# Kernel optimization log

Measured on AMD Instinct MI355X. Metric: run time of the kernel, lower is better.

Reference implementation:

```python
import jax, jax.numpy as jnp
import numpy as np

DILATIONS = (1, 2, 4, 8, 16, 32, 64, 128, 256, 512)
K = 3            # kernel_size
CH = 128         # channels
B, T = 4, 16384
L = len(DILATIONS)


def _conv1x1(x, w, b=None):
    # x: [B, Cin, T], w: [Cout, Cin, 1] -> [B, Cout, T]
    y = jnp.einsum('oc,bct->bot', w[..., 0], x)
    return y if b is None else y + b[None, :, None]


def _causal_dilated_conv(x, w, b, d):
    # buffer of zeros of size (K-1)*d concatenated on the left == causal left pad
    pad = (K - 1) * d
    y = jax.lax.conv_general_dilated(
        x, w, window_strides=(1,), padding=[(pad, 0)], rhs_dilation=(d,),
        dimension_numbers=('NCH', 'OIH', 'NCH'))
    return y + b[None, :, None]


def setup_inputs() -> dict:
    key = jax.random.key(0)
    ks = jax.random.split(key, 12)
    s = 0.1  # keep gated activations out of saturation
    return {
        'x': jax.random.normal(ks[0], (B, 1, T), jnp.float32),
        'c': jax.random.normal(ks[1], (B, 1, T), jnp.float32),
        'head_init': jnp.zeros((B, CH, T), jnp.float32),
        'w_re': jax.random.normal(ks[2], (CH, 1, 1), jnp.float32) * s,
        'conv_w': jax.random.normal(ks[3], (L, 2 * CH, CH, K), jnp.float32) * s,
        'conv_b': jax.random.normal(ks[4], (L, 2 * CH), jnp.float32) * s,
        'mix_w': jax.random.normal(ks[5], (L, 2 * CH, 1, 1), jnp.float32) * s,
        'w1x1': jax.random.normal(ks[6], (L, CH, CH, 1), jnp.float32) * s,
        'b1x1': jax.random.normal(ks[7], (L, CH), jnp.float32) * s,
        'w_head': jax.random.normal(ks[8], (1, CH, 1), jnp.float32) * s,
        'b_head': jax.random.normal(ks[9], (1,), jnp.float32) * s,
    }


def reference(x, c, head_init, w_re, conv_w, conv_b, mix_w, w1x1, b1x1, w_head, b_head):
    h = _conv1x1(x, w_re)               # rechannel: [B, CH, T]
    head = head_init                    # head accumulator (zeros == head_input=None)
    for li, d in enumerate(DILATIONS):  # fixed small layer loop (structurally distinct dilations)
        z = _causal_dilated_conv(h, conv_w[li], conv_b[li], d)   # [B, 2CH, T]
        z = z + _conv1x1(c, mix_w[li])                           # conditioning mixer
        post = jnp.tanh(z[:, :CH]) * jax.nn.sigmoid(z[:, CH:])   # gated activation
        h = h + _conv1x1(post, w1x1[li], b1x1[li])               # residual
        head = head + post
    out = _conv1x1(head, w_head, b_head)  # [B, 1, T]
    return out, h
```

## Files before the change

kernel.cpp:

```cpp
#include <hip/hip_runtime.h>
#include <hip/hip_bf16.h>

#define B_   4
#define T_   16384
#define CH_  128
#define TCH_ 256
#define NL_  10
#define TT_  64
#define SHW_ 196
#define SPW_ 68

typedef __attribute__((ext_vector_type(8))) short short8;
typedef __attribute__((ext_vector_type(4))) float f32x4;

#define MFMA16(a, b, c) __builtin_amdgcn_mfma_f32_16x16x32_bf16(a, b, c, 0, 0, 0)

__device__ __forceinline__ unsigned short f2bf(float f) {
  unsigned u = __float_as_uint(f);
  return (unsigned short)((u + 0x7FFFu + ((u >> 16) & 1u)) >> 16);
}
__device__ __forceinline__ float bf2f(unsigned s) {
  return __uint_as_float((s & 0xFFFFu) << 16);
}
__device__ __forceinline__ float fast_tanh(float x) {
  float e = __expf(2.0f * fabsf(x));
  float t = 1.0f - 2.0f / (e + 1.0f);
  return copysignf(t, x);
}
__device__ __forceinline__ float fast_sig(float x) {
  return 1.0f / (1.0f + __expf(-x));
}

__global__ __launch_bounds__(256) void pack_w(
    const float* __restrict__ conv_w, const float* __restrict__ w1x1,
    unsigned short* __restrict__ wpackA, unsigned short* __restrict__ wpack1) {
  const int NA = NL_ * 4 * 4 * 12 * 64 * 8;
  int idx = blockIdx.x * 256 + threadIdx.x;
  if (idx < NA) {
    int j = idx & 7;
    int t1 = idx >> 3;
    int l = t1 & 63;
    int t2 = t1 >> 6;
    int ks = t2 % 12;
    int t3 = t2 / 12;
    int f = t3 & 3;
    int t4 = t3 >> 2;
    int w = t4 & 3;
    int li = t4 >> 2;
    int o = 32 * w + 16 * (f & 1) + 128 * (f >> 1) + (l & 15);
    int ck = 32 * ks + 8 * (l >> 4) + j;
    int c = ck & 127, k = ck >> 7;
    wpackA[idx] = f2bf(conv_w[((li * TCH_ + o) * CH_ + c) * 3 + k]);
  } else {
    int i2 = idx - NA;
    if (i2 < NL_ * 4 * 2 * 4 * 64 * 8) {
      int j = i2 & 7;
      int t1 = i2 >> 3;
      int l = t1 & 63;
      int t2 = t1 >> 6;
      int ks = t2 & 3;
      int t3 = t2 >> 2;
      int p = t3 & 1;
      int t4 = t3 >> 1;
      int w = t4 & 3;
      int li = t4 >> 2;
      int o = 32 * w + 16 * p + (l & 15);
      int c = 32 * ks + 8 * (l >> 4) + j;
      wpack1[i2] = f2bf(w1x1[(li * CH_ + o) * CH_ + c]);
    }
  }
}

__global__ __launch_bounds__(256) void rechannel_k(
    const float* __restrict__ x, const float* __restrict__ w_re,
    unsigned short* __restrict__ hb) {
  int flat = blockIdx.x * 256 + threadIdx.x;
  int cid = flat & 15;
  int t = (flat >> 4) & (T_ - 1);
  int b = flat >> 18;
  float xv = x[b * T_ + t];
  const float* wr = w_re + cid * 8;
  union { short8 s; unsigned short u[8]; } o;
#pragma unroll
  for (int j = 0; j < 8; ++j) o.u[j] = f2bf(wr[j] * xv);
  *(short8*)(hb + (size_t)(b * T_ + t) * CH_ + cid * 8) = o.s;
}

__global__ __launch_bounds__(256) void out_init_k(
    const float* __restrict__ head_init, const float* __restrict__ w_head,
    const float* __restrict__ b_head, float* __restrict__ out) {
  int idx = blockIdx.x * 256 + threadIdx.x;
  int b = idx / T_;
  int t = idx - b * T_;
  float acc = b_head[0];
#pragma unroll 8
  for (int c = 0; c < CH_; ++c)
    acc += w_head[c] * head_init[(b * CH_ + c) * T_ + t];
  out[idx] = acc;
}

__global__ __launch_bounds__(256, 2) void layer_k(
    const unsigned short* __restrict__ hin,
    unsigned short* __restrict__ hob,
    float* __restrict__ hof,
    const float* __restrict__ cin, float* __restrict__ out,
    const unsigned short* __restrict__ wA,
    const unsigned short* __restrict__ w1p,
    const float* __restrict__ bconv,
    const float* __restrict__ wmix,
    const float* __restrict__ b1,
    const float* __restrict__ w_head,
    int d, int is_final) {
  __shared__ unsigned shH[TT_ * SHW_];
  __shared__ unsigned shP[TT_ * SPW_];
  __shared__ float shR[4 * 4 * 16];

  const int tid = threadIdx.x;
  const int b = blockIdx.y;
  const int t0 = blockIdx.x * TT_;

#pragma unroll
  for (int it = 0; it < 12; ++it) {
    int flat = it * 256 + tid;
    int cid = flat & 15;
    int tt = (flat >> 4) & 63;
    int k = flat >> 10;
    int t = t0 + tt - (2 - k) * d;
    uint4 v = make_uint4(0u, 0u, 0u, 0u);
    if (t >= 0)
      v = *(const uint4*)(hin + ((size_t)(b * T_ + t) * CH_ + cid * 8));
    *(uint4*)(shH + tt * SHW_ + k * 64 + cid * 4) = v;
  }
  __syncthreads();

  const int wave = __builtin_amdgcn_readfirstlane(tid >> 6);
  const int lane = tid & 63;
  const int r = lane & 15;
  const int g = lane >> 4;

  f32x4 accL[2][4], accH[2][4];
#pragma unroll
  for (int p = 0; p < 2; ++p)
#pragma unroll
    for (int q = 0; q < 4; ++q) {
      accL[p][q] = (f32x4){0.f, 0.f, 0.f, 0.f};
      accH[p][q] = (f32x4){0.f, 0.f, 0.f, 0.f};
    }

  const short8* wAv = (const short8*)wA;
#pragma unroll
  for (int ks = 0; ks < 12; ++ks) {
    short8 bf[4];
#pragma unroll
    for (int q = 0; q < 4; ++q)
      bf[q] = *(const short8*)(shH + (16 * q + r) * SHW_ + 16 * ks + 4 * g);
    short8 a0 = wAv[((wave * 4 + 0) * 12 + ks) * 64 + lane];
    short8 a1 = wAv[((wave * 4 + 1) * 12 + ks) * 64 + lane];
    short8 a2 = wAv[((wave * 4 + 2) * 12 + ks) * 64 + lane];
    short8 a3 = wAv[((wave * 4 + 3) * 12 + ks) * 64 + lane];
#pragma unroll
    for (int q = 0; q < 4; ++q) {
      accL[0][q] = MFMA16(a0, bf[q], accL[0][q]);
      accL[1][q] = MFMA16(a1, bf[q], accL[1][q]);
      accH[0][q] = MFMA16(a2, bf[q], accH[0][q]);
      accH[1][q] = MFMA16(a3, bf[q], accH[1][q]);
    }
  }

  float cq[4];
#pragma unroll
  for (int q = 0; q < 4; ++q) cq[q] = cin[b * T_ + t0 + 16 * q + r];

  float hs[4] = {0.f, 0.f, 0.f, 0.f};
#pragma unroll
  for (int p = 0; p < 2; ++p) {
    float bcL[4], bcH[4], wmL[4], wmH[4], whv[4];
#pragma unroll
    for (int j = 0; j < 4; ++j) {
      int o = 32 * wave + 16 * p + 4 * g + j;
      bcL[j] = bconv[o];
      bcH[j] = bconv[o + CH_];
      wmL[j] = wmix[o];
      wmH[j] = wmix[o + CH_];
      whv[j] = w_head[o];
    }
#pragma unroll
    for (int q = 0; q < 4; ++q) {
      float pv[4];
#pragma unroll
      for (int j = 0; j < 4; ++j) {
        float zl = accL[p][q][j] + bcL[j] + wmL[j] * cq[q];
        float zh = accH[p][q][j] + bcH[j] + wmH[j] * cq[q];
        pv[j] = fast_tanh(zl) * fast_sig(zh);
        hs[q] += whv[j] * pv[j];
      }
      uint2 pk;
      pk.x = (unsigned)f2bf(pv[0]) | ((unsigned)f2bf(pv[1]) << 16);
      pk.y = (unsigned)f2bf(pv[2]) | ((unsigned)f2bf(pv[3]) << 16);
      *(uint2*)(shP + (16 * q + r) * SPW_ + 16 * wave + 8 * p + 2 * g) = pk;
    }
  }
  __syncthreads();

  f32x4 acc2[2][4];
#pragma unroll
  for (int p = 0; p < 2; ++p)
#pragma unroll
    for (int q = 0; q < 4; ++q) acc2[p][q] = (f32x4){0.f, 0.f, 0.f, 0.f};

  const short8* w1v = (const short8*)w1p;
#pragma unroll
  for (int ks = 0; ks < 4; ++ks) {
    short8 bp[4];
#pragma unroll
    for (int q = 0; q < 4; ++q)
      bp[q] = *(const short8*)(shP + (16 * q + r) * SPW_ + 16 * ks + 4 * g);
    short8 a0 = w1v[((wave * 2 + 0) * 4 + ks) * 64 + lane];
    short8 a1 = w1v[((wave * 2 + 1) * 4 + ks) * 64 + lane];
#pragma unroll
    for (int q = 0; q < 4; ++q) {
      acc2[0][q] = MFMA16(a0, bp[q], acc2[0][q]);
      acc2[1][q] = MFMA16(a1, bp[q], acc2[1][q]);
    }
  }

  float res[2][4][4];
  const int o0b = 32 * wave + 4 * g;
#pragma unroll
  for (int p = 0; p < 2; ++p) {
    const int o0 = o0b + 16 * p;
    float b1v[4];
#pragma unroll
    for (int j = 0; j < 4; ++j) b1v[j] = b1[o0 + j];
#pragma unroll
    for (int q = 0; q < 4; ++q) {
      uint2 hv = *(const uint2*)(shH + (16 * q + r) * SHW_ + 128 + (o0 >> 1));
      res[p][q][0] = bf2f(hv.x) + b1v[0] + acc2[p][q][0];
      res[p][q][1] = bf2f(hv.x >> 16) + b1v[1] + acc2[p][q][1];
      res[p][q][2] = bf2f(hv.y) + b1v[2] + acc2[p][q][2];
      res[p][q][3] = bf2f(hv.y >> 16) + b1v[3] + acc2[p][q][3];
    }
  }

#pragma unroll
  for (int q = 0; q < 4; ++q) {
    hs[q] += __shfl_xor(hs[q], 16);
    hs[q] += __shfl_xor(hs[q], 32);
  }
  if (g == 0) {
#pragma unroll
    for (int q = 0; q < 4; ++q) shR[(wave * 4 + q) * 16 + r] = hs[q];
  }
  __syncthreads();

  if (tid < 64) {
    int q = tid >> 4, rr = tid & 15;
    float tot = shR[(0 * 4 + q) * 16 + rr] + shR[(1 * 4 + q) * 16 + rr] +
                shR[(2 * 4 + q) * 16 + rr] + shR[(3 * 4 + q) * 16 + rr];
    out[b * T_ + t0 + 16 * q + rr] += tot;
  }

  if (!is_final) {
#pragma unroll
    for (int p = 0; p < 2; ++p) {
      const int o0 = o0b + 16 * p;
#pragma unroll
      for (int q = 0; q < 4; ++q) {
        uint2 pk;
        pk.x = (unsigned)f2bf(res[p][q][0]) | ((unsigned)f2bf(res[p][q][1]) << 16);
        pk.y = (unsigned)f2bf(res[p][q][2]) | ((unsigned)f2bf(res[p][q][3]) << 16);
        *(uint2*)(shH + (16 * q + r) * SHW_ + (o0 >> 1)) = pk;
      }
    }
    __syncthreads();
#pragma unroll
    for (int it = 0; it < 4; ++it) {
      int flat = it * 256 + tid;
      int cid = flat & 15;
      int tt = flat >> 4;
      *(uint4*)(hob + ((size_t)(b * T_ + t0 + tt) * CH_ + cid * 8)) =
          *(const uint4*)(shH + tt * SHW_ + cid * 4);
    }
  } else {
#pragma unroll
    for (int p = 0; p < 2; ++p) {
      const int o0 = o0b + 16 * p;
#pragma unroll
      for (int q = 0; q < 4; ++q) {
#pragma unroll
        for (int j = 0; j < 4; ++j)
          hof[(size_t)(b * CH_ + o0 + j) * T_ + t0 + 16 * q + r] = res[p][q][j];
      }
    }
  }
}

extern "C" void kernel_launch(void* const* d_in, const int* in_sizes, int n_in,
                              void* d_out, int out_size, void* d_ws, size_t ws_size,
                              hipStream_t stream) {
  const float* x         = (const float*)d_in[0];
  const float* c         = (const float*)d_in[1];
  const float* head_init = (const float*)d_in[2];
  const float* w_re      = (const float*)d_in[3];
  const float* conv_w    = (const float*)d_in[4];
  const float* conv_b    = (const float*)d_in[5];
  const float* mix_w     = (const float*)d_in[6];
  const float* w1x1      = (const float*)d_in[7];
  const float* b1x1      = (const float*)d_in[8];
  const float* w_head    = (const float*)d_in[9];
  const float* b_head    = (const float*)d_in[10];

  float* out = (float*)d_out;
  float* hof = out + B_ * T_;

  unsigned short* hb0 = (unsigned short*)d_ws;
  unsigned short* hb1 = hb0 + (size_t)B_ * T_ * CH_;
  unsigned short* wpackA = hb1 + (size_t)B_ * T_ * CH_;
  unsigned short* wpack1 = wpackA + NL_ * 4 * 4 * 12 * 64 * 8;

  const int n_pack = NL_ * 4 * 4 * 12 * 64 * 8 + NL_ * 4 * 2 * 4 * 64 * 8;
  pack_w<<<(n_pack + 255) / 256, 256, 0, stream>>>(conv_w, w1x1, wpackA, wpack1);

  rechannel_k<<<(B_ * T_ * 16) / 256, 256, 0, stream>>>(x, w_re, hb0);
  out_init_k<<<(B_ * T_) / 256, 256, 0, stream>>>(head_init, w_head, b_head, out);

  const int dil[NL_] = {1, 2, 4, 8, 16, 32, 64, 128, 256, 512};
  for (int li = 0; li < NL_; ++li) {
    const unsigned short* hin = (li & 1) ? hb1 : hb0;
    unsigned short* hob       = (li & 1) ? hb0 : hb1;
    int is_final = (li == NL_ - 1);
    layer_k<<<dim3(T_ / TT_, B_), 256, 0, stream>>>(
        hin, hob, hof, c, out,
        wpackA + li * (4 * 4 * 12 * 64 * 8),
        wpack1 + li * (4 * 2 * 4 * 64 * 8),
        conv_b + li * TCH_,
        mix_w + li * TCH_,
        b1x1 + li * CH_,
        w_head,
        dil[li], is_final);
  }
}
```

Baseline: 324.7 us.

## Double layer time tile to 128 with 512-thread blocks and per-wave channel split

The layer kernel now processes 128 time steps per block with 8 waves instead of 64 steps with 4 waves. Each wave owns 16 output channels across all eight 16-step time tiles. The goal is to halve global weight-fragment traffic per output and to halve the number of blocks. In exchange, LDS use per block roughly doubles, so likely only one block fits per CU. Each wave also reads more LDS B-fragments per MFMA, which could make LDS bandwidth the bottleneck.

Measured after the change: 365.7 us. 1.13x slower.

```diff
diff --git a/kernel.cpp b/kernel.cpp
--- a/kernel.cpp
+++ b/kernel.cpp
@@ -6,7 +6,7 @@
 #define CH_  128
 #define TCH_ 256
 #define NL_  10
-#define TT_  64
+#define TTL_ 128
 #define SHW_ 196
 #define SPW_ 68
 
@@ -99,7 +99,7 @@
   out[idx] = acc;
 }
 
-__global__ __launch_bounds__(256, 2) void layer_k(
+__global__ __launch_bounds__(512, 2) void layer_k(
     const unsigned short* __restrict__ hin,
     unsigned short* __restrict__ hob,
     float* __restrict__ hof,
@@ -111,20 +111,20 @@
     const float* __restrict__ b1,
     const float* __restrict__ w_head,
     int d, int is_final) {
-  __shared__ unsigned shH[TT_ * SHW_];
-  __shared__ unsigned shP[TT_ * SPW_];
-  __shared__ float shR[4 * 4 * 16];
+  __shared__ unsigned shH[TTL_ * SHW_];
+  __shared__ unsigned shP[TTL_ * SPW_];
+  __shared__ float shR[8 * 8 * 16];
 
   const int tid = threadIdx.x;
   const int b = blockIdx.y;
-  const int t0 = blockIdx.x * TT_;
+  const int t0 = blockIdx.x * TTL_;
 
 #pragma unroll
   for (int it = 0; it < 12; ++it) {
-    int flat = it * 256 + tid;
+    int flat = it * 512 + tid;
     int cid = flat & 15;
-    int tt = (flat >> 4) & 63;
-    int k = flat >> 10;
+    int tt = (flat >> 4) & 127;
+    int k = flat >> 11;
     int t = t0 + tt - (2 - k) * d;
     uint4 v = make_uint4(0u, 0u, 0u, 0u);
     if (t >= 0)
@@ -137,145 +137,121 @@
   const int lane = tid & 63;
   const int r = lane & 15;
   const int g = lane >> 4;
-
-  f32x4 accL[2][4], accH[2][4];
-#pragma unroll
-  for (int p = 0; p < 2; ++p)
-#pragma unroll
-    for (int q = 0; q < 4; ++q) {
-      accL[p][q] = (f32x4){0.f, 0.f, 0.f, 0.f};
-      accH[p][q] = (f32x4){0.f, 0.f, 0.f, 0.f};
-    }
+  const int wlo = (wave >> 1) * 4 + (wave & 1);
+
+  f32x4 accLo[8], accHi[8];
+#pragma unroll
+  for (int q = 0; q < 8; ++q) {
+    accLo[q] = (f32x4){0.f, 0.f, 0.f, 0.f};
+    accHi[q] = (f32x4){0.f, 0.f, 0.f, 0.f};
+  }
 
   const short8* wAv = (const short8*)wA;
 #pragma unroll
   for (int ks = 0; ks < 12; ++ks) {
-    short8 bf[4];
-#pragma unroll
-    for (int q = 0; q < 4; ++q)
+    short8 bf[8];
+#pragma unroll
+    for (int q = 0; q < 8; ++q)
       bf[q] = *(const short8*)(shH + (16 * q + r) * SHW_ + 16 * ks + 4 * g);
-    short8 a0 = wAv[((wave * 4 + 0) * 12 + ks) * 64 + lane];
-    short8 a1 = wAv[((wave * 4 + 1) * 12 + ks) * 64 + lane];
-    short8 a2 = wAv[((wave * 4 + 2) * 12 + ks) * 64 + lane];
-    short8 a3 = wAv[((wave * 4 + 3) * 12 + ks) * 64 + lane];
-#pragma unroll
-    for (int q = 0; q < 4; ++q) {
-      accL[0][q] = MFMA16(a0, bf[q], accL[0][q]);
-      accL[1][q] = MFMA16(a1, bf[q], accL[1][q]);
-      accH[0][q] = MFMA16(a2, bf[q], accH[0][q]);
-      accH[1][q] = MFMA16(a3, bf[q], accH[1][q]);
-    }
-  }
-
-  float cq[4];
-#pragma unroll
-  for (int q = 0; q < 4; ++q) cq[q] = cin[b * T_ + t0 + 16 * q + r];
-
-  float hs[4] = {0.f, 0.f, 0.f, 0.f};
-#pragma unroll
-  for (int p = 0; p < 2; ++p) {
-    float bcL[4], bcH[4], wmL[4], wmH[4], whv[4];
+    short8 alo = wAv[(wlo * 12 + ks) * 64 + lane];
+    short8 ahi = wAv[((wlo + 2) * 12 + ks) * 64 + lane];
+#pragma unroll
+    for (int q = 0; q < 8; ++q) {
+      accLo[q] = MFMA16(alo, bf[q], accLo[q]);
+      accHi[q] = MFMA16(ahi, bf[q], accHi[q]);
+    }
+  }
+
+  float bcL[4], bcH[4], wmL[4], wmH[4], whv[4];
+#pragma unroll
+  for (int j = 0; j < 4; ++j) {
+    int o = 16 * wave + 4 * g + j;
+    bcL[j] = bconv[o];
+    bcH[j] = bconv[o + CH_];
+    wmL[j] = wmix[o];
+    wmH[j] = wmix[o + CH_];
+    whv[j] = w_head[o];
+  }
+
+  float hs[8];
+#pragma unroll
+  for (int q = 0; q < 8; ++q) {
+    float cq = cin[b * T_ + t0 + 16 * q + r];
+    float pv[4];
 #pragma unroll
     for (int j = 0; j < 4; ++j) {
-      int o = 32 * wave + 16 * p + 4 * g + j;
-      bcL[j] = bconv[o];
-      bcH[j] = bconv[o + CH_];
-      wmL[j] = wmix[o];
-      wmH[j] = wmix[o + CH_];
-      whv[j] = w_head[o];
-    }
-#pragma unroll
-    for (int q = 0; q < 4; ++q) {
-      float pv[4];
-#pragma unroll
-      for (int j = 0; j < 4; ++j) {
-        float zl = accL[p][q][j] + bcL[j] + wmL[j] * cq[q];
-        float zh = accH[p][q][j] + bcH[j] + wmH[j] * cq[q];
-        pv[j] = fast_tanh(zl) * fast_sig(zh);
-        hs[q] += whv[j] * pv[j];
-      }
-      uint2 pk;
-      pk.x = (unsigned)f2bf(pv[0]) | ((unsigned)f2bf(pv[1]) << 16);
-      pk.y = (unsigned)f2bf(pv[2]) | ((unsigned)f2bf(pv[3]) << 16);
-      *(uint2*)(shP + (16 * q + r) * SPW_ + 16 * wave + 8 * p + 2 * g) = pk;
-    }
+      float zl = accLo[q][j] + bcL[j] + wmL[j] * cq;
+      float zh = accHi[q][j] + bcH[j] + wmH[j] * cq;
+      pv[j] = fast_tanh(zl) * fast_sig(zh);
+    }
+    hs[q] = whv[0] * pv[0] + whv[1] * pv[1] + whv[2] * pv[2] + whv[3] * pv[3];
+    uint2 pk;
+    pk.x = (unsigned)f2bf(pv[0]) | ((unsigned)f2bf(pv[1]) << 16);
+    pk.y = (unsigned)f2bf(pv[2]) | ((unsigned)f2bf(pv[3]) << 16);
+    *(uint2*)(shP + (16 * q + r) * SPW_ + 8 * wave + 2 * g) = pk;
   }
   __syncthreads();
 
-  f32x4 acc2[2][4];
-#pragma unroll
-  for (int p = 0; p < 2; ++p)
-#pragma unroll
-    for (int q = 0; q < 4; ++q) acc2[p][q] = (f32x4){0.f, 0.f, 0.f, 0.f};
+  f32x4 acc2[8];
+#pragma unroll
+  for (int q = 0; q < 8; ++q) acc2[q] = (f32x4){0.f, 0.f, 0.f, 0.f};
 
   const short8* w1v = (const short8*)w1p;
 #pragma unroll
   for (int ks = 0; ks < 4; ++ks) {
-    short8 bp[4];
-#pragma unroll
-    for (int q = 0; q < 4; ++q)
+    short8 bp[8];
+#pragma unroll
+    for (int q = 0; q < 8; ++q)
       bp[q] = *(const short8*)(shP + (16 * q + r) * SPW_ + 16 * ks + 4 * g);
-    short8 a0 = w1v[((wave * 2 + 0) * 4 + ks) * 64 + lane];
-    short8 a1 = w1v[((wave * 2 + 1) * 4 + ks) * 64 + lane];
-#pragma unroll
-    for (int q = 0; q < 4; ++q) {
-      acc2[0][q] = MFMA16(a0, bp[q], acc2[0][q]);
-      acc2[1][q] = MFMA16(a1, bp[q], acc2[1][q]);
-    }
-  }
-
-  float res[2][4][4];
-  const int o0b = 32 * wave + 4 * g;
-#pragma unroll
-  for (int p = 0; p < 2; ++p) {
-    const int o0 = o0b + 16 * p;
-    float b1v[4];
-#pragma unroll
-    for (int j = 0; j < 4; ++j) b1v[j] = b1[o0 + j];
-#pragma unroll
-    for (int q = 0; q < 4; ++q) {
-      uint2 hv = *(const uint2*)(shH + (16 * q + r) * SHW_ + 128 + (o0 >> 1));
-      res[p][q][0] = bf2f(hv.x) + b1v[0] + acc2[p][q][0];
-      res[p][q][1] = bf2f(hv.x >> 16) + b1v[1] + acc2[p][q][1];
-      res[p][q][2] = bf2f(hv.y) + b1v[2] + acc2[p][q][2];
-      res[p][q][3] = bf2f(hv.y >> 16) + b1v[3] + acc2[p][q][3];
-    }
-  }
-
-#pragma unroll
-  for (int q = 0; q < 4; ++q) {
+    short8 a1 = w1v[(wave * 4 + ks) * 64 + lane];
+#pragma unroll
+    for (int q = 0; q < 8; ++q) acc2[q] = MFMA16(a1, bp[q], acc2[q]);
+  }
+
+  float res[8][4];
+  float b1v[4];
+#pragma unroll
+  for (int j = 0; j < 4; ++j) b1v[j] = b1[16 * wave + 4 * g + j];
+#pragma unroll
+  for (int q = 0; q < 8; ++q) {
+    uint2 hv = *(const uint2*)(shH + (16 * q + r) * SHW_ + 128 + 8 * wave + 2 * g);
+    res[q][0] = bf2f(hv.x) + b1v[0] + acc2[q][0];
+    res[q][1] = bf2f(hv.x >> 16) + b1v[1] + acc2[q][1];
+    res[q][2] = bf2f(hv.y) + b1v[2] + acc2[q][2];
+    res[q][3] = bf2f(hv.y >> 16) + b1v[3] + acc2[q][3];
+  }
+
+#pragma unroll
+  for (int q = 0; q < 8; ++q) {
     hs[q] += __shfl_xor(hs[q], 16);
     hs[q] += __shfl_xor(hs[q], 32);
   }
   if (g == 0) {
 #pragma unroll
-    for (int q = 0; q < 4; ++q) shR[(wave * 4 + q) * 16 + r] = hs[q];
+    for (int q = 0; q < 8; ++q) shR[(wave * 8 + q) * 16 + r] = hs[q];
   }
   __syncthreads();
 
-  if (tid < 64) {
+  if (tid < 128) {
     int q = tid >> 4, rr = tid & 15;
-    float tot = shR[(0 * 4 + q) * 16 + rr] + shR[(1 * 4 + q) * 16 + rr] +
-                shR[(2 * 4 + q) * 16 + rr] + shR[(3 * 4 + q) * 16 + rr];
+    float tot = 0.f;
+#pragma unroll
+    for (int w = 0; w < 8; ++w) tot += shR[(w * 8 + q) * 16 + rr];
     out[b * T_ + t0 + 16 * q + rr] += tot;
   }
 
   if (!is_final) {
 #pragma unroll
-    for (int p = 0; p < 2; ++p) {
-      const int o0 = o0b + 16 * p;
-#pragma unroll
-      for (int q = 0; q < 4; ++q) {
-        uint2 pk;
-        pk.x = (unsigned)f2bf(res[p][q][0]) | ((unsigned)f2bf(res[p][q][1]) << 16);
-        pk.y = (unsigned)f2bf(res[p][q][2]) | ((unsigned)f2bf(res[p][q][3]) << 16);
-        *(uint2*)(shH + (16 * q + r) * SHW_ + (o0 >> 1)) = pk;
-      }
+    for (int q = 0; q < 8; ++q) {
+      uint2 pk;
+      pk.x = (unsigned)f2bf(res[q][0]) | ((unsigned)f2bf(res[q][1]) << 16);
+      pk.y = (unsigned)f2bf(res[q][2]) | ((unsigned)f2bf(res[q][3]) << 16);
+      *(uint2*)(shH + (16 * q + r) * SHW_ + 8 * wave + 2 * g) = pk;
     }
     __syncthreads();
 #pragma unroll
     for (int it = 0; it < 4; ++it) {
-      int flat = it * 256 + tid;
+      int flat = it * 512 + tid;
       int cid = flat & 15;
       int tt = flat >> 4;
       *(uint4*)(hob + ((size_t)(b * T_ + t0 + tt) * CH_ + cid * 8)) =
@@ -283,14 +259,11 @@
     }
   } else {
 #pragma unroll
-    for (int p = 0; p < 2; ++p) {
-      const int o0 = o0b + 16 * p;
-#pragma unroll
-      for (int q = 0; q < 4; ++q) {
-#pragma unroll
-        for (int j = 0; j < 4; ++j)
-          hof[(size_t)(b * CH_ + o0 + j) * T_ + t0 + 16 * q + r] = res[p][q][j];
-      }
+    for (int q = 0; q < 8; ++q) {
+#pragma unroll
+      for (int j = 0; j < 4; ++j)
+        hof[(size_t)(b * CH_ + 16 * wave + 4 * g + j) * T_ + t0 + 16 * q + r] =
+            res[q][j];
     }
   }
 }
@@ -329,7 +302,7 @@
     const unsigned short* hin = (li & 1) ? hb1 : hb0;
     unsigned short* hob       = (li & 1) ? hb0 : hb1;
     int is_final = (li == NL_ - 1);
-    layer_k<<<dim3(T_ / TT_, B_), 256, 0, stream>>>(
+    layer_k<<<dim3(T_ / TTL_, B_), 512, 0, stream>>>(
         hin, hob, hof, c, out,
         wpackA + li * (4 * 4 * 12 * 64 * 8),
         wpack1 + li * (4 * 2 * 4 * 64 * 8),
```
